# Kernel optimization log

Hardware: AMD Instinct MI355X
Metric: run time of the kernel (lower is better)

The kernel has to match this reference:

```python
import jax, jax.numpy as jnp
import numpy as np


def setup_inputs() -> dict:
    key = jax.random.key(0)
    ks = jax.random.split(key, 8)
    B, C, W = 8, 512, 2048
    Cq = C // 8
    sq = 1.0 / np.sqrt(C)
    return {
        "x": jax.random.normal(ks[0], (B, C, W), dtype=jnp.float32),
        "Wq": jax.random.normal(ks[1], (Cq, C), dtype=jnp.float32) * sq,
        "bq": jax.random.normal(ks[2], (Cq,), dtype=jnp.float32) * 0.01,
        "Wk": jax.random.normal(ks[3], (Cq, C), dtype=jnp.float32) * sq,
        "bk": jax.random.normal(ks[4], (Cq,), dtype=jnp.float32) * 0.01,
        "Wv": jax.random.normal(ks[5], (C, C), dtype=jnp.float32) * sq,
        "bv": jax.random.normal(ks[6], (C,), dtype=jnp.float32) * 0.01,
        "gamma": jax.random.normal(ks[7], (1,), dtype=jnp.float32),
    }


def reference(x, Wq, bq, Wk, bk, Wv, bv, gamma):
    # x: [B, C, W]; 1x1 Conv1d == channel-mixing matmul.
    q = jnp.einsum("qc,bcw->bqw", Wq, x) + bq[None, :, None]   # [B, C/8, W]
    k = jnp.einsum("qc,bcw->bqw", Wk, x) + bk[None, :, None]   # [B, C/8, W]
    v = jnp.einsum("oc,bcw->bow", Wv, x) + bv[None, :, None]   # [B, C, W]
    # energy[b, i, j] = sum_q q[b, q, i] * k[b, q, j]  (query positions i attend over j)
    energy = jnp.einsum("bqi,bqj->bij", q, k)                  # [B, W, W]
    attn = jax.nn.softmax(energy, axis=-1)                     # [B, W, W]
    # out[b, c, i] = sum_j v[b, c, j] * attn[b, i, j]
    out = jnp.einsum("bcj,bij->bci", v, attn)                  # [B, C, W]
    return gamma[0] * out + x
```

## Files before the change

### kernel.cpp

```cpp
#include <hip/hip_runtime.h>

#define B_  8
#define C_  512
#define CQ_ 64
#define W_  2048
#define NROW 640

typedef __attribute__((ext_vector_type(8))) short  short8;
typedef __attribute__((ext_vector_type(4))) float  f32x4;
typedef unsigned short ushort;
typedef unsigned long long ull;

static constexpr size_t OFF_Q  = 0;
static constexpr size_t OFF_K  = OFF_Q  + (size_t)B_ * CQ_ * W_;
static constexpr size_t OFF_VB = OFF_K  + (size_t)B_ * CQ_ * W_;
static constexpr size_t OFF_E  = OFF_VB + (size_t)B_ * C_ * W_ / 2;
static constexpr size_t OFF_M  = OFF_E  + (size_t)B_ * W_ * W_;
static constexpr size_t OFF_S  = OFF_M  + (size_t)B_ * W_;
static constexpr size_t OFF_XTH = OFF_E;
static constexpr size_t OFF_XTL = OFF_XTH + (size_t)B_ * W_ * C_ / 2;
static constexpr size_t OFF_WH  = OFF_XTL + (size_t)B_ * W_ * C_ / 2;
static constexpr size_t OFF_WL  = OFF_WH  + (size_t)NROW * C_ / 2;

static __device__ __forceinline__ ushort f2bf(float f) {
    unsigned int u = __builtin_bit_cast(unsigned int, f);
    u += 0x7fffu + ((u >> 16) & 1u);
    return (ushort)(u >> 16);
}
static __device__ __forceinline__ float bf2f(ushort h) {
    unsigned int u = ((unsigned int)h) << 16;
    return __builtin_bit_cast(float, u);
}
static __device__ __forceinline__ ull pack4(const ushort* p) {
    return (ull)p[0] | ((ull)p[1] << 16) | ((ull)p[2] << 32) | ((ull)p[3] << 48);
}

__global__ __launch_bounds__(256) void k_wsplit(
    const float* __restrict__ Wq, const float* __restrict__ Wk,
    const float* __restrict__ Wv, ushort* __restrict__ wh, ushort* __restrict__ wl)
{
    const int idx = (blockIdx.x * 256 + threadIdx.x) * 4;
    const int row = idx >> 9, col = idx & 511;
    const float* src;
    if (row < 64)       src = Wq + (size_t)row * C_ + col;
    else if (row < 128) src = Wk + (size_t)(row - 64) * C_ + col;
    else                src = Wv + (size_t)(row - 128) * C_ + col;
    float4 v = *reinterpret_cast<const float4*>(src);
    float vv[4] = {v.x, v.y, v.z, v.w};
    ushort h[4], lo[4];
    #pragma unroll
    for (int j = 0; j < 4; ++j) {
        h[j]  = f2bf(vv[j]);
        lo[j] = f2bf(vv[j] - bf2f(h[j]));
    }
    *reinterpret_cast<ull*>(wh + idx) = pack4(h);
    *reinterpret_cast<ull*>(wl + idx) = pack4(lo);
}

__global__ __launch_bounds__(256) void k_xt(
    const float* __restrict__ x, ushort* __restrict__ xth, ushort* __restrict__ xtl)
{
    const int b = blockIdx.z, c0 = blockIdx.y * 64, w0 = blockIdx.x * 64;
    __shared__ float ts[64][65];
    const int t = threadIdx.x;
    #pragma unroll
    for (int m = 0; m < 4; ++m) {
        int fi = m * 256 + t;
        int c = fi >> 4, c4 = fi & 15;
        float4 v = *reinterpret_cast<const float4*>(x + ((size_t)b * C_ + c0 + c) * W_ + w0 + c4 * 4);
        ts[c][c4 * 4 + 0] = v.x; ts[c][c4 * 4 + 1] = v.y;
        ts[c][c4 * 4 + 2] = v.z; ts[c][c4 * 4 + 3] = v.w;
    }
    __syncthreads();
    #pragma unroll
    for (int m = 0; m < 4; ++m) {
        int w  = m * 16 + (t >> 4);
        int cc = (t & 15) * 4;
        ushort h[4], lo[4];
        #pragma unroll
        for (int j = 0; j < 4; ++j) {
            float v = ts[cc + j][w];
            h[j]  = f2bf(v);
            lo[j] = f2bf(v - bf2f(h[j]));
        }
        size_t base = ((size_t)b * W_ + w0 + w) * C_ + c0 + cc;
        *reinterpret_cast<ull*>(xth + base) = pack4(h);
        *reinterpret_cast<ull*>(xtl + base) = pack4(lo);
    }
}

__global__ __launch_bounds__(512) void k_projm(
    const ushort* __restrict__ wh, const ushort* __restrict__ wl,
    const ushort* __restrict__ xth, const ushort* __restrict__ xtl,
    const float* __restrict__ bq, const float* __restrict__ bk,
    const float* __restrict__ bv,
    float* __restrict__ qo, float* __restrict__ ko, ushort* __restrict__ vb)
{
    const int b = blockIdx.y, w0 = blockIdx.x * 64;
    const int t = threadIdx.x, l = t & 63, wid = t >> 6;
    const int lr = l & 15, lkb = (l >> 4) * 8;

    f32x4 acc[5][4];
    #pragma unroll
    for (int m = 0; m < 5; ++m)
        #pragma unroll
        for (int n = 0; n < 4; ++n) acc[m][n] = (f32x4){0.f, 0.f, 0.f, 0.f};

    const size_t xbase = ((size_t)b * W_ + w0 + lr) * C_ + lkb;

    for (int kc = 0; kc < 16; ++kc) {
        short8 bhf[4], blf[4];
        #pragma unroll
        for (int n = 0; n < 4; ++n) {
            bhf[n] = *reinterpret_cast<const short8*>(xth + xbase + (size_t)n * 16 * C_ + kc * 32);
            blf[n] = *reinterpret_cast<const short8*>(xtl + xbase + (size_t)n * 16 * C_ + kc * 32);
        }
        #pragma unroll
        for (int m = 0; m < 5; ++m) {
            const int arow = (wid + m * 8) * 16 + lr;
            const size_t abase = (size_t)arow * C_ + kc * 32 + lkb;
            short8 ah = *reinterpret_cast<const short8*>(wh + abase);
            #pragma unroll
            for (int n = 0; n < 4; ++n)
                acc[m][n] = __builtin_amdgcn_mfma_f32_16x16x32_bf16(ah, bhf[n], acc[m][n], 0, 0, 0);
            if (m == 0) {
                short8 al = *reinterpret_cast<const short8*>(wl + abase);
                #pragma unroll
                for (int n = 0; n < 4; ++n) {
                    acc[m][n] = __builtin_amdgcn_mfma_f32_16x16x32_bf16(al, bhf[n], acc[m][n], 0, 0, 0);
                    acc[m][n] = __builtin_amdgcn_mfma_f32_16x16x32_bf16(ah, blf[n], acc[m][n], 0, 0, 0);
                }
            }
        }
    }

    #pragma unroll
    for (int m = 0; m < 5; ++m) {
        const int rbase16 = (wid + m * 8) * 16;
        #pragma unroll
        for (int n = 0; n < 4; ++n) {
            const int wcol = w0 + n * 16 + lr;
            #pragma unroll
            for (int r = 0; r < 4; ++r) {
                const int row = rbase16 + (l >> 4) * 4 + r;
                float val = acc[m][n][r];
                if (rbase16 < 64) {
                    val += bq[row];
                    qo[((size_t)b * CQ_ + row) * W_ + wcol] = val;
                } else if (rbase16 < 128) {
                    const int rl = row - 64;
                    val += bk[rl];
                    ko[((size_t)b * CQ_ + rl) * W_ + wcol] = val;
                } else {
                    const int rl = row - 128;
                    val += bv[rl];
                    vb[((size_t)b * C_ + rl) * W_ + wcol] = f2bf(val);
                }
            }
        }
    }
}

__global__ __launch_bounds__(256) void k_energy(
    const float* __restrict__ q, const float* __restrict__ k, float* __restrict__ E)
{
    const int b  = blockIdx.z;
    const int i0 = blockIdx.y * 128;
    const int j0 = blockIdx.x * 128;

    __shared__ __align__(16) float qs[64][132];
    __shared__ __align__(16) float ks[64][132];

    const int t  = threadIdx.x;
    const int tx = t & 15, ty = t >> 4;

    const float* qsrc = q + (size_t)b * CQ_ * W_ + i0;
    const float* ksrc = k + (size_t)b * CQ_ * W_ + j0;
    #pragma unroll
    for (int m = 0; m < 8; ++m) {
        int fi = m * 256 + t;
        int qq = fi >> 5;
        int iq = fi & 31;
        *reinterpret_cast<float4*>(&qs[qq][iq * 4]) =
            *reinterpret_cast<const float4*>(qsrc + (size_t)qq * W_ + iq * 4);
        *reinterpret_cast<float4*>(&ks[qq][iq * 4]) =
            *reinterpret_cast<const float4*>(ksrc + (size_t)qq * W_ + iq * 4);
    }
    __syncthreads();

    float acc[8][8];
    #pragma unroll
    for (int i = 0; i < 8; ++i)
        #pragma unroll
        for (int j = 0; j < 8; ++j) acc[i][j] = 0.f;

    #pragma unroll 8
    for (int kk = 0; kk < 64; ++kk) {
        float4 qa = *reinterpret_cast<const float4*>(&qs[kk][ty * 4]);
        float4 qb = *reinterpret_cast<const float4*>(&qs[kk][64 + ty * 4]);
        float4 ka = *reinterpret_cast<const float4*>(&ks[kk][tx * 4]);
        float4 kb = *reinterpret_cast<const float4*>(&ks[kk][64 + tx * 4]);
        float qv[8] = {qa.x, qa.y, qa.z, qa.w, qb.x, qb.y, qb.z, qb.w};
        float kv[8] = {ka.x, ka.y, ka.z, ka.w, kb.x, kb.y, kb.z, kb.w};
        #pragma unroll
        for (int i = 0; i < 8; ++i)
            #pragma unroll
            for (int j = 0; j < 8; ++j)
                acc[i][j] = fmaf(qv[i], kv[j], acc[i][j]);
    }

    float* erow0 = E + ((size_t)b * W_ + i0) * W_ + j0;
    #pragma unroll
    for (int ih = 0; ih < 8; ++ih) {
        int ii = ((ih & 4) << 4) + ty * 4 + (ih & 3);
        float* er = erow0 + (size_t)ii * W_;
        float4 o0 = make_float4(acc[ih][0], acc[ih][1], acc[ih][2], acc[ih][3]);
        float4 o1 = make_float4(acc[ih][4], acc[ih][5], acc[ih][6], acc[ih][7]);
        *reinterpret_cast<float4*>(er + tx * 4) = o0;
        *reinterpret_cast<float4*>(er + 64 + tx * 4) = o1;
    }
}

__global__ __launch_bounds__(256) void k_stats(const float* __restrict__ E,
                                               float* __restrict__ mrow,
                                               float* __restrict__ srow)
{
    const int i = blockIdx.x;
    const int b = blockIdx.y;
    const float* row = E + ((size_t)b * W_ + i) * W_;
    const int t = threadIdx.x;

    float v8[8];
    float lm = -3.0e38f;
    #pragma unroll
    for (int m = 0; m < 8; ++m) {
        v8[m] = row[m * 256 + t];
        lm = fmaxf(lm, v8[m]);
    }
    #pragma unroll
    for (int off = 32; off >= 1; off >>= 1)
        lm = fmaxf(lm, __shfl_xor(lm, off));

    __shared__ float red[8];
    const int wv = t >> 6;
    if ((t & 63) == 0) red[wv] = lm;
    __syncthreads();
    const float bm = fmaxf(fmaxf(red[0], red[1]), fmaxf(red[2], red[3]));

    float ls = 0.f;
    #pragma unroll
    for (int m = 0; m < 8; ++m) ls += __expf(v8[m] - bm);
    #pragma unroll
    for (int off = 32; off >= 1; off >>= 1)
        ls += __shfl_xor(ls, off);
    if ((t & 63) == 0) red[4 + wv] = ls;
    __syncthreads();
    if (t == 0) {
        const float bs = red[4] + red[5] + red[6] + red[7];
        mrow[(size_t)b * W_ + i] = bm;
        srow[(size_t)b * W_ + i] = 1.0f / bs;
    }
}

__global__ __launch_bounds__(256) void k_pv(
    const ushort* __restrict__ vb, const float* __restrict__ E,
    const float* __restrict__ mrow, const float* __restrict__ srow,
    const float* __restrict__ x, const float* __restrict__ gamma,
    float* __restrict__ out)
{
    const int b  = blockIdx.z;
    const int c0 = blockIdx.y * 128;
    const int i0 = blockIdx.x * 128;

    __shared__ __align__(16) ushort Vt[128 * 64];
    __shared__ __align__(16) ushort Pt[128 * 64];

    const int t = threadIdx.x, l = t & 63, wid = t >> 6;
    const int wi = wid & 1, wc = wid >> 1;
    const int lr = l & 15, lk = (l >> 4) * 8;

    int srow4[4], scc4[4];
    float mi4[4], si4[4];
    #pragma unroll
    for (int m = 0; m < 4; ++m) {
        int fi = m * 256 + t;
        srow4[m] = fi >> 3;
        scc4[m]  = fi & 7;
        mi4[m] = mrow[(size_t)b * W_ + i0 + srow4[m]];
        si4[m] = srow[(size_t)b * W_ + i0 + srow4[m]];
    }

    int idxA[4][2], idxB[4][2];
    #pragma unroll
    for (int f = 0; f < 4; ++f)
        #pragma unroll
        for (int kc = 0; kc < 2; ++kc) {
            int rowA = wc * 64 + f * 16 + lr;
            int rowB = wi * 64 + f * 16 + lr;
            idxA[f][kc] = ((rowA * 64) + kc * 32 + lk) ^ ((rowA & 7) << 3);
            idxB[f][kc] = ((rowB * 64) + kc * 32 + lk) ^ ((rowB & 7) << 3);
        }

    f32x4 acc[4][4];
    #pragma unroll
    for (int i = 0; i < 4; ++i)
        #pragma unroll
        for (int j = 0; j < 4; ++j) acc[i][j] = (f32x4){0.f, 0.f, 0.f, 0.f};

    const ushort* vbase = vb + ((size_t)b * C_ + c0) * W_;
    const float*  ebase = E + ((size_t)b * W_ + i0) * W_;

    for (int jt = 0; jt < 32; ++jt) {
        const int j0 = jt * 64;
        #pragma unroll
        for (int m = 0; m < 4; ++m) {
            int row = srow4[m], cc = scc4[m];
            short8 v8 = *reinterpret_cast<const short8*>(vbase + (size_t)row * W_ + j0 + cc * 8);
            int idx = ((row * 64) + cc * 8) ^ ((row & 7) << 3);
            *reinterpret_cast<short8*>(&Vt[idx]) = v8;
        }
        #pragma unroll
        for (int m = 0; m < 4; ++m) {
            int row = srow4[m], cc = scc4[m];
            int idx = ((row * 64) + cc * 8) ^ ((row & 7) << 3);
            const float* eb = ebase + (size_t)row * W_ + j0 + cc * 8;
            float4 e0 = *reinterpret_cast<const float4*>(eb);
            float4 e1 = *reinterpret_cast<const float4*>(eb + 4);
            float mi = mi4[m], si = si4[m];
            short8 ps;
            ps[0] = (short)f2bf(__expf(e0.x - mi) * si);
            ps[1] = (short)f2bf(__expf(e0.y - mi) * si);
            ps[2] = (short)f2bf(__expf(e0.z - mi) * si);
            ps[3] = (short)f2bf(__expf(e0.w - mi) * si);
            ps[4] = (short)f2bf(__expf(e1.x - mi) * si);
            ps[5] = (short)f2bf(__expf(e1.y - mi) * si);
            ps[6] = (short)f2bf(__expf(e1.z - mi) * si);
            ps[7] = (short)f2bf(__expf(e1.w - mi) * si);
            *reinterpret_cast<short8*>(&Pt[idx]) = ps;
        }
        __syncthreads();
        #pragma unroll
        for (int kc = 0; kc < 2; ++kc) {
            short8 a[4], p[4];
            #pragma unroll
            for (int f = 0; f < 4; ++f) {
                a[f] = *reinterpret_cast<const short8*>(&Vt[idxA[f][kc]]);
                p[f] = *reinterpret_cast<const short8*>(&Pt[idxB[f][kc]]);
            }
            #pragma unroll
            for (int fc = 0; fc < 4; ++fc)
                #pragma unroll
                for (int fi = 0; fi < 4; ++fi)
                    acc[fc][fi] = __builtin_amdgcn_mfma_f32_16x16x32_bf16(a[fc], p[fi], acc[fc][fi], 0, 0, 0);
        }
        __syncthreads();
    }

    const float g = gamma[0];
    #pragma unroll
    for (int fc = 0; fc < 4; ++fc) {
        int c = c0 + wc * 64 + fc * 16 + (l >> 4) * 4;
        #pragma unroll
        for (int fi = 0; fi < 4; ++fi) {
            int icol = i0 + wi * 64 + fi * 16 + lr;
            #pragma unroll
            for (int r = 0; r < 4; ++r) {
                size_t addr = ((size_t)b * C_ + c + r) * W_ + icol;
                out[addr] = g * acc[fc][fi][r] + x[addr];
            }
        }
    }
}

extern "C" void kernel_launch(void* const* d_in, const int* in_sizes, int n_in,
                              void* d_out, int out_size, void* d_ws, size_t ws_size,
                              hipStream_t stream)
{
    const float* x     = (const float*)d_in[0];
    const float* Wq    = (const float*)d_in[1];
    const float* bq    = (const float*)d_in[2];
    const float* Wk    = (const float*)d_in[3];
    const float* bk    = (const float*)d_in[4];
    const float* Wv    = (const float*)d_in[5];
    const float* bv    = (const float*)d_in[6];
    const float* gamma = (const float*)d_in[7];
    float* out = (float*)d_out;
    float* ws  = (float*)d_ws;

    float*  q    = ws + OFF_Q;
    float*  k    = ws + OFF_K;
    ushort* vbf  = (ushort*)(ws + OFF_VB);
    float*  E    = ws + OFF_E;
    float*  mrow = ws + OFF_M;
    float*  srow = ws + OFF_S;
    ushort* xth  = (ushort*)(ws + OFF_XTH);
    ushort* xtl  = (ushort*)(ws + OFF_XTL);
    ushort* wh   = (ushort*)(ws + OFF_WH);
    ushort* wl   = (ushort*)(ws + OFF_WL);

    hipLaunchKernelGGL(k_wsplit, dim3(NROW * C_ / 1024, 1, 1), dim3(256), 0, stream,
                       Wq, Wk, Wv, wh, wl);
    hipLaunchKernelGGL(k_xt,     dim3(W_ / 64, C_ / 64, B_), dim3(256), 0, stream,
                       x, xth, xtl);
    hipLaunchKernelGGL(k_projm,  dim3(W_ / 64, B_, 1), dim3(512), 0, stream,
                       wh, wl, xth, xtl, bq, bk, bv, q, k, vbf);
    hipLaunchKernelGGL(k_energy, dim3(W_ / 128, W_ / 128, B_), dim3(256), 0, stream,
                       q, k, E);
    hipLaunchKernelGGL(k_stats,  dim3(W_, B_, 1), dim3(256), 0, stream,
                       E, mrow, srow);
    hipLaunchKernelGGL(k_pv,     dim3(W_ / 128, C_ / 128, B_), dim3(256), 0, stream,
                       vbf, E, mrow, srow, x, gamma, out);
}
```

Before: 299.3 us.

## Fuse energy, softmax and PV into a single flash-attention kernel

Replaces the separate energy GEMM, row-stats pass and PV kernel with one online-softmax flash kernel that never writes the W×W energy matrix to global memory. Q and K are now emitted by the projection kernel as transposed bf16 hi/lo split pairs, and QK^T is computed with three MFMAs per step to approximate fp32 precision. V is read straight from global memory rather than staged in LDS, and only 4 of 8 waves compute the scores, which may leave compute underused and serialise the softmax against the PV MFMAs. The grid drops to 256 blocks of 512 threads, each covering all 512 channels for 64 query rows.

Result: slower. 314.5 us (+5.1%).

```diff
diff --git a/kernel.cpp b/kernel.cpp
--- a/kernel.cpp
+++ b/kernel.cpp
@@ -11,13 +11,12 @@
 typedef unsigned short ushort;
 typedef unsigned long long ull;
 
-static constexpr size_t OFF_Q  = 0;
-static constexpr size_t OFF_K  = OFF_Q  + (size_t)B_ * CQ_ * W_;
-static constexpr size_t OFF_VB = OFF_K  + (size_t)B_ * CQ_ * W_;
-static constexpr size_t OFF_E  = OFF_VB + (size_t)B_ * C_ * W_ / 2;
-static constexpr size_t OFF_M  = OFF_E  + (size_t)B_ * W_ * W_;
-static constexpr size_t OFF_S  = OFF_M  + (size_t)B_ * W_;
-static constexpr size_t OFF_XTH = OFF_E;
+static constexpr size_t OFF_VB  = 0;
+static constexpr size_t OFF_QTH = OFF_VB  + (size_t)B_ * C_ * W_ / 2;
+static constexpr size_t OFF_QTL = OFF_QTH + (size_t)B_ * W_ * CQ_ / 2;
+static constexpr size_t OFF_KTH = OFF_QTL + (size_t)B_ * W_ * CQ_ / 2;
+static constexpr size_t OFF_KTL = OFF_KTH + (size_t)B_ * W_ * CQ_ / 2;
+static constexpr size_t OFF_XTH = OFF_KTL + (size_t)B_ * W_ * CQ_ / 2;
 static constexpr size_t OFF_XTL = OFF_XTH + (size_t)B_ * W_ * C_ / 2;
 static constexpr size_t OFF_WH  = OFF_XTL + (size_t)B_ * W_ * C_ / 2;
 static constexpr size_t OFF_WL  = OFF_WH  + (size_t)NROW * C_ / 2;
@@ -94,7 +93,9 @@
     const ushort* __restrict__ xth, const ushort* __restrict__ xtl,
     const float* __restrict__ bq, const float* __restrict__ bk,
     const float* __restrict__ bv,
-    float* __restrict__ qo, float* __restrict__ ko, ushort* __restrict__ vb)
+    ushort* __restrict__ qth, ushort* __restrict__ qtl,
+    ushort* __restrict__ kth, ushort* __restrict__ ktl,
+    ushort* __restrict__ vb)
 {
     const int b = blockIdx.y, w0 = blockIdx.x * 64;
     const int t = threadIdx.x, l = t & 63, wid = t >> 6;
@@ -137,169 +138,66 @@
     #pragma unroll
     for (int m = 0; m < 5; ++m) {
         const int rbase16 = (wid + m * 8) * 16;
-        #pragma unroll
-        for (int n = 0; n < 4; ++n) {
-            const int wcol = w0 + n * 16 + lr;
-            #pragma unroll
-            for (int r = 0; r < 4; ++r) {
-                const int row = rbase16 + (l >> 4) * 4 + r;
-                float val = acc[m][n][r];
-                if (rbase16 < 64) {
-                    val += bq[row];
-                    qo[((size_t)b * CQ_ + row) * W_ + wcol] = val;
-                } else if (rbase16 < 128) {
-                    const int rl = row - 64;
-                    val += bk[rl];
-                    ko[((size_t)b * CQ_ + rl) * W_ + wcol] = val;
-                } else {
-                    const int rl = row - 128;
-                    val += bv[rl];
-                    vb[((size_t)b * C_ + rl) * W_ + wcol] = f2bf(val);
-                }
-            }
-        }
-    }
-}
-
-__global__ __launch_bounds__(256) void k_energy(
-    const float* __restrict__ q, const float* __restrict__ k, float* __restrict__ E)
-{
-    const int b  = blockIdx.z;
-    const int i0 = blockIdx.y * 128;
-    const int j0 = blockIdx.x * 128;
-
-    __shared__ __align__(16) float qs[64][132];
-    __shared__ __align__(16) float ks[64][132];
-
-    const int t  = threadIdx.x;
-    const int tx = t & 15, ty = t >> 4;
-
-    const float* qsrc = q + (size_t)b * CQ_ * W_ + i0;
-    const float* ksrc = k + (size_t)b * CQ_ * W_ + j0;
-    #pragma unroll
-    for (int m = 0; m < 8; ++m) {
-        int fi = m * 256 + t;
-        int qq = fi >> 5;
-        int iq = fi & 31;
-        *reinterpret_cast<float4*>(&qs[qq][iq * 4]) =
-            *reinterpret_cast<const float4*>(qsrc + (size_t)qq * W_ + iq * 4);
-        *reinterpret_cast<float4*>(&ks[qq][iq * 4]) =
-            *reinterpret_cast<const float4*>(ksrc + (size_t)qq * W_ + iq * 4);
-    }
-    __syncthreads();
-
-    float acc[8][8];
-    #pragma unroll
-    for (int i = 0; i < 8; ++i)
-        #pragma unroll
-        for (int j = 0; j < 8; ++j) acc[i][j] = 0.f;
-
-    #pragma unroll 8
-    for (int kk = 0; kk < 64; ++kk) {
-        float4 qa = *reinterpret_cast<const float4*>(&qs[kk][ty * 4]);
-        float4 qb = *reinterpret_cast<const float4*>(&qs[kk][64 + ty * 4]);
-        float4 ka = *reinterpret_cast<const float4*>(&ks[kk][tx * 4]);
-        float4 kb = *reinterpret_cast<const float4*>(&ks[kk][64 + tx * 4]);
-        float qv[8] = {qa.x, qa.y, qa.z, qa.w, qb.x, qb.y, qb.z, qb.w};
-        float kv[8] = {ka.x, ka.y, ka.z, ka.w, kb.x, kb.y, kb.z, kb.w};
-        #pragma unroll
-        for (int i = 0; i < 8; ++i)
-            #pragma unroll
-            for (int j = 0; j < 8; ++j)
-                acc[i][j] = fmaf(qv[i], kv[j], acc[i][j]);
-    }
-
-    float* erow0 = E + ((size_t)b * W_ + i0) * W_ + j0;
-    #pragma unroll
-    for (int ih = 0; ih < 8; ++ih) {
-        int ii = ((ih & 4) << 4) + ty * 4 + (ih & 3);
-        float* er = erow0 + (size_t)ii * W_;
-        float4 o0 = make_float4(acc[ih][0], acc[ih][1], acc[ih][2], acc[ih][3]);
-        float4 o1 = make_float4(acc[ih][4], acc[ih][5], acc[ih][6], acc[ih][7]);
-        *reinterpret_cast<float4*>(er + tx * 4) = o0;
-        *reinterpret_cast<float4*>(er + 64 + tx * 4) = o1;
-    }
-}
-
-__global__ __launch_bounds__(256) void k_stats(const float* __restrict__ E,
-                                               float* __restrict__ mrow,
-                                               float* __restrict__ srow)
-{
-    const int i = blockIdx.x;
-    const int b = blockIdx.y;
-    const float* row = E + ((size_t)b * W_ + i) * W_;
-    const int t = threadIdx.x;
-
-    float v8[8];
-    float lm = -3.0e38f;
-    #pragma unroll
-    for (int m = 0; m < 8; ++m) {
-        v8[m] = row[m * 256 + t];
-        lm = fmaxf(lm, v8[m]);
-    }
-    #pragma unroll
-    for (int off = 32; off >= 1; off >>= 1)
-        lm = fmaxf(lm, __shfl_xor(lm, off));
-
-    __shared__ float red[8];
-    const int wv = t >> 6;
-    if ((t & 63) == 0) red[wv] = lm;
-    __syncthreads();
-    const float bm = fmaxf(fmaxf(red[0], red[1]), fmaxf(red[2], red[3]));
-
-    float ls = 0.f;
-    #pragma unroll
-    for (int m = 0; m < 8; ++m) ls += __expf(v8[m] - bm);
-    #pragma unroll
-    for (int off = 32; off >= 1; off >>= 1)
-        ls += __shfl_xor(ls, off);
-    if ((t & 63) == 0) red[4 + wv] = ls;
-    __syncthreads();
-    if (t == 0) {
-        const float bs = red[4] + red[5] + red[6] + red[7];
-        mrow[(size_t)b * W_ + i] = bm;
-        srow[(size_t)b * W_ + i] = 1.0f / bs;
-    }
-}
-
-__global__ __launch_bounds__(256) void k_pv(
-    const ushort* __restrict__ vb, const float* __restrict__ E,
-    const float* __restrict__ mrow, const float* __restrict__ srow,
+        if (rbase16 < 128) {
+            ushort* oh = (rbase16 < 64) ? qth : kth;
+            ushort* ol = (rbase16 < 64) ? qtl : ktl;
+            const float* bias = (rbase16 < 64) ? bq : bk;
+            const int rb = rbase16 & 63;
+            #pragma unroll
+            for (int n = 0; n < 4; ++n) {
+                const int wcol = w0 + n * 16 + lr;
+                ushort h4[4], l4[4];
+                #pragma unroll
+                for (int r = 0; r < 4; ++r) {
+                    const int rowl = rb + (l >> 4) * 4 + r;
+                    float val = acc[m][n][r] + bias[rowl];
+                    h4[r] = f2bf(val);
+                    l4[r] = f2bf(val - bf2f(h4[r]));
+                }
+                size_t base = ((size_t)b * W_ + wcol) * CQ_ + rb + (l >> 4) * 4;
+                *reinterpret_cast<ull*>(oh + base) = pack4(h4);
+                *reinterpret_cast<ull*>(ol + base) = pack4(l4);
+            }
+        } else {
+            #pragma unroll
+            for (int n = 0; n < 4; ++n) {
+                const int wcol = w0 + n * 16 + lr;
+                #pragma unroll
+                for (int r = 0; r < 4; ++r) {
+                    const int rl = rbase16 - 128 + (l >> 4) * 4 + r;
+                    vb[((size_t)b * C_ + rl) * W_ + wcol] = f2bf(acc[m][n][r] + bv[rl]);
+                }
+            }
+        }
+    }
+}
+
+__global__ __launch_bounds__(512) void k_flash(
+    const ushort* __restrict__ qth, const ushort* __restrict__ qtl,
+    const ushort* __restrict__ kth, const ushort* __restrict__ ktl,
+    const ushort* __restrict__ vb,
     const float* __restrict__ x, const float* __restrict__ gamma,
     float* __restrict__ out)
 {
-    const int b  = blockIdx.z;
-    const int c0 = blockIdx.y * 128;
-    const int i0 = blockIdx.x * 128;
-
-    __shared__ __align__(16) ushort Vt[128 * 64];
-    __shared__ __align__(16) ushort Pt[128 * 64];
-
+    const int b  = blockIdx.y;
+    const int i0 = blockIdx.x * 64;
     const int t = threadIdx.x, l = t & 63, wid = t >> 6;
-    const int wi = wid & 1, wc = wid >> 1;
-    const int lr = l & 15, lk = (l >> 4) * 8;
-
-    int srow4[4], scc4[4];
-    float mi4[4], si4[4];
-    #pragma unroll
-    for (int m = 0; m < 4; ++m) {
-        int fi = m * 256 + t;
-        srow4[m] = fi >> 3;
-        scc4[m]  = fi & 7;
-        mi4[m] = mrow[(size_t)b * W_ + i0 + srow4[m]];
-        si4[m] = srow[(size_t)b * W_ + i0 + srow4[m]];
-    }
-
-    int idxA[4][2], idxB[4][2];
-    #pragma unroll
-    for (int f = 0; f < 4; ++f)
+    const int lr = l & 15, lkb = (l >> 4) * 8;
+    const int ib = (wid & 3) * 16;
+
+    __shared__ __align__(16) ushort Ps[64 * 64];
+    __shared__ float scale_lds[64];
+    __shared__ float l_lds[64];
+
+    short8 qh[2], ql[2];
+    if (wid < 4) {
+        const size_t qbase = ((size_t)b * W_ + i0 + ib + lr) * CQ_ + lkb;
         #pragma unroll
         for (int kc = 0; kc < 2; ++kc) {
-            int rowA = wc * 64 + f * 16 + lr;
-            int rowB = wi * 64 + f * 16 + lr;
-            idxA[f][kc] = ((rowA * 64) + kc * 32 + lk) ^ ((rowA & 7) << 3);
-            idxB[f][kc] = ((rowB * 64) + kc * 32 + lk) ^ ((rowB & 7) << 3);
-        }
+            qh[kc] = *reinterpret_cast<const short8*>(qth + qbase + kc * 32);
+            ql[kc] = *reinterpret_cast<const short8*>(qtl + qbase + kc * 32);
+        }
+    }
 
     f32x4 acc[4][4];
     #pragma unroll
@@ -307,45 +205,100 @@
         #pragma unroll
         for (int j = 0; j < 4; ++j) acc[i][j] = (f32x4){0.f, 0.f, 0.f, 0.f};
 
-    const ushort* vbase = vb + ((size_t)b * C_ + c0) * W_;
-    const float*  ebase = E + ((size_t)b * W_ + i0) * W_;
+    float mrun[4] = {-3.0e38f, -3.0e38f, -3.0e38f, -3.0e38f};
+    float lrun[4] = {0.f, 0.f, 0.f, 0.f};
+
+    const ushort* vbase = vb + ((size_t)b * C_ + wid * 64) * W_;
 
     for (int jt = 0; jt < 32; ++jt) {
         const int j0 = jt * 64;
-        #pragma unroll
-        for (int m = 0; m < 4; ++m) {
-            int row = srow4[m], cc = scc4[m];
-            short8 v8 = *reinterpret_cast<const short8*>(vbase + (size_t)row * W_ + j0 + cc * 8);
-            int idx = ((row * 64) + cc * 8) ^ ((row & 7) << 3);
-            *reinterpret_cast<short8*>(&Vt[idx]) = v8;
-        }
-        #pragma unroll
-        for (int m = 0; m < 4; ++m) {
-            int row = srow4[m], cc = scc4[m];
-            int idx = ((row * 64) + cc * 8) ^ ((row & 7) << 3);
-            const float* eb = ebase + (size_t)row * W_ + j0 + cc * 8;
-            float4 e0 = *reinterpret_cast<const float4*>(eb);
-            float4 e1 = *reinterpret_cast<const float4*>(eb + 4);
-            float mi = mi4[m], si = si4[m];
-            short8 ps;
-            ps[0] = (short)f2bf(__expf(e0.x - mi) * si);
-            ps[1] = (short)f2bf(__expf(e0.y - mi) * si);
-            ps[2] = (short)f2bf(__expf(e0.z - mi) * si);
-            ps[3] = (short)f2bf(__expf(e0.w - mi) * si);
-            ps[4] = (short)f2bf(__expf(e1.x - mi) * si);
-            ps[5] = (short)f2bf(__expf(e1.y - mi) * si);
-            ps[6] = (short)f2bf(__expf(e1.z - mi) * si);
-            ps[7] = (short)f2bf(__expf(e1.w - mi) * si);
-            *reinterpret_cast<short8*>(&Pt[idx]) = ps;
+
+        if (wid < 4) {
+            f32x4 e[4];
+            #pragma unroll
+            for (int n = 0; n < 4; ++n) e[n] = (f32x4){0.f, 0.f, 0.f, 0.f};
+            #pragma unroll
+            for (int kc = 0; kc < 2; ++kc) {
+                short8 bh[4], bl[4];
+                #pragma unroll
+                for (int n = 0; n < 4; ++n) {
+                    const size_t ka = ((size_t)b * W_ + j0 + n * 16 + lr) * CQ_ + kc * 32 + lkb;
+                    bh[n] = *reinterpret_cast<const short8*>(kth + ka);
+                    bl[n] = *reinterpret_cast<const short8*>(ktl + ka);
+                }
+                #pragma unroll
+                for (int n = 0; n < 4; ++n) {
+                    e[n] = __builtin_amdgcn_mfma_f32_16x16x32_bf16(qh[kc], bh[n], e[n], 0, 0, 0);
+                    e[n] = __builtin_amdgcn_mfma_f32_16x16x32_bf16(ql[kc], bh[n], e[n], 0, 0, 0);
+                    e[n] = __builtin_amdgcn_mfma_f32_16x16x32_bf16(qh[kc], bl[n], e[n], 0, 0, 0);
+                }
+            }
+            float rmax[4];
+            #pragma unroll
+            for (int r = 0; r < 4; ++r)
+                rmax[r] = fmaxf(fmaxf(e[0][r], e[1][r]), fmaxf(e[2][r], e[3][r]));
+            #pragma unroll
+            for (int off = 1; off <= 8; off <<= 1)
+                #pragma unroll
+                for (int r = 0; r < 4; ++r)
+                    rmax[r] = fmaxf(rmax[r], __shfl_xor(rmax[r], off));
+            float sc[4];
+            #pragma unroll
+            for (int r = 0; r < 4; ++r) {
+                const float mnew = fmaxf(mrun[r], rmax[r]);
+                sc[r] = __expf(mrun[r] - mnew);
+                mrun[r] = mnew;
+            }
+            float rsum[4] = {0.f, 0.f, 0.f, 0.f};
+            #pragma unroll
+            for (int n = 0; n < 4; ++n)
+                #pragma unroll
+                for (int r = 0; r < 4; ++r) {
+                    const float p = __expf(e[n][r] - mrun[r]);
+                    e[n][r] = p;
+                    rsum[r] += p;
+                }
+            #pragma unroll
+            for (int off = 1; off <= 8; off <<= 1)
+                #pragma unroll
+                for (int r = 0; r < 4; ++r)
+                    rsum[r] += __shfl_xor(rsum[r], off);
+            #pragma unroll
+            for (int r = 0; r < 4; ++r)
+                lrun[r] = lrun[r] * sc[r] + rsum[r];
+            #pragma unroll
+            for (int n = 0; n < 4; ++n)
+                #pragma unroll
+                for (int r = 0; r < 4; ++r) {
+                    const int row = ib + (l >> 4) * 4 + r;
+                    const int idx = (row * 64 + n * 16 + lr) ^ ((row & 7) << 3);
+                    Ps[idx] = f2bf(e[n][r]);
+                }
+            if (lr == 0) {
+                #pragma unroll
+                for (int r = 0; r < 4; ++r)
+                    scale_lds[ib + (l >> 4) * 4 + r] = sc[r];
+            }
         }
         __syncthreads();
+
+        float s4[4];
+        #pragma unroll
+        for (int fi = 0; fi < 4; ++fi) s4[fi] = scale_lds[fi * 16 + lr];
+        #pragma unroll
+        for (int fc = 0; fc < 4; ++fc)
+            #pragma unroll
+            for (int fi = 0; fi < 4; ++fi)
+                acc[fc][fi] *= s4[fi];
         #pragma unroll
         for (int kc = 0; kc < 2; ++kc) {
             short8 a[4], p[4];
             #pragma unroll
             for (int f = 0; f < 4; ++f) {
-                a[f] = *reinterpret_cast<const short8*>(&Vt[idxA[f][kc]]);
-                p[f] = *reinterpret_cast<const short8*>(&Pt[idxB[f][kc]]);
+                a[f] = *reinterpret_cast<const short8*>(vbase + (size_t)(f * 16 + lr) * W_ + j0 + kc * 32 + lkb);
+                const int row = f * 16 + lr;
+                const int idx = ((row * 64) + kc * 32 + lkb) ^ ((row & 7) << 3);
+                p[f] = *reinterpret_cast<const short8*>(&Ps[idx]);
             }
             #pragma unroll
             for (int fc = 0; fc < 4; ++fc)
@@ -356,17 +309,27 @@
         __syncthreads();
     }
 
+    if (wid < 4 && lr == 0) {
+        #pragma unroll
+        for (int r = 0; r < 4; ++r)
+            l_lds[ib + (l >> 4) * 4 + r] = lrun[r];
+    }
+    __syncthreads();
+    float linv[4];
+    #pragma unroll
+    for (int fi = 0; fi < 4; ++fi) linv[fi] = 1.0f / l_lds[fi * 16 + lr];
+
     const float g = gamma[0];
     #pragma unroll
     for (int fc = 0; fc < 4; ++fc) {
-        int c = c0 + wc * 64 + fc * 16 + (l >> 4) * 4;
+        const int c = wid * 64 + fc * 16 + (l >> 4) * 4;
         #pragma unroll
         for (int fi = 0; fi < 4; ++fi) {
-            int icol = i0 + wi * 64 + fi * 16 + lr;
+            const int icol = i0 + fi * 16 + lr;
             #pragma unroll
             for (int r = 0; r < 4; ++r) {
-                size_t addr = ((size_t)b * C_ + c + r) * W_ + icol;
-                out[addr] = g * acc[fc][fi][r] + x[addr];
+                const size_t addr = ((size_t)b * C_ + c + r) * W_ + icol;
+                out[addr] = g * acc[fc][fi][r] * linv[fi] + x[addr];
             }
         }
     }
@@ -387,27 +350,22 @@
     float* out = (float*)d_out;
     float* ws  = (float*)d_ws;
 
-    float*  q    = ws + OFF_Q;
-    float*  k    = ws + OFF_K;
-    ushort* vbf  = (ushort*)(ws + OFF_VB);
-    float*  E    = ws + OFF_E;
-    float*  mrow = ws + OFF_M;
-    float*  srow = ws + OFF_S;
-    ushort* xth  = (ushort*)(ws + OFF_XTH);
-    ushort* xtl  = (ushort*)(ws + OFF_XTL);
-    ushort* wh   = (ushort*)(ws + OFF_WH);
-    ushort* wl   = (ushort*)(ws + OFF_WL);
+    ushort* vbf = (ushort*)(ws + OFF_VB);
+    ushort* qth = (ushort*)(ws + OFF_QTH);
+    ushort* qtl = (ushort*)(ws + OFF_QTL);
+    ushort* kth = (ushort*)(ws + OFF_KTH);
+    ushort* ktl = (ushort*)(ws + OFF_KTL);
+    ushort* xth = (ushort*)(ws + OFF_XTH);
+    ushort* xtl = (ushort*)(ws + OFF_XTL);
+    ushort* wh  = (ushort*)(ws + OFF_WH);
+    ushort* wl  = (ushort*)(ws + OFF_WL);
 
     hipLaunchKernelGGL(k_wsplit, dim3(NROW * C_ / 1024, 1, 1), dim3(256), 0, stream,
                        Wq, Wk, Wv, wh, wl);
     hipLaunchKernelGGL(k_xt,     dim3(W_ / 64, C_ / 64, B_), dim3(256), 0, stream,
                        x, xth, xtl);
     hipLaunchKernelGGL(k_projm,  dim3(W_ / 64, B_, 1), dim3(512), 0, stream,
-                       wh, wl, xth, xtl, bq, bk, bv, q, k, vbf);
-    hipLaunchKernelGGL(k_energy, dim3(W_ / 128, W_ / 128, B_), dim3(256), 0, stream,
-                       q, k, E);
-    hipLaunchKernelGGL(k_stats,  dim3(W_, B_, 1), dim3(256), 0, stream,
-                       E, mrow, srow);
-    hipLaunchKernelGGL(k_pv,     dim3(W_ / 128, C_ / 128, B_), dim3(256), 0, stream,
-                       vbf, E, mrow, srow, x, gamma, out);
-}
+                       wh, wl, xth, xtl, bq, bk, bv, qth, qtl, kth, ktl, vbf);
+    hipLaunchKernelGGL(k_flash,  dim3(W_ / 64, B_, 1), dim3(512), 0, stream,
+                       qth, qtl, kth, ktl, vbf, x, gamma, out);
+}
```
